# Kernel optimization log

Hardware: AMD Instinct MI355X
Metric: run time of the kernel (lower is better)

Reference implementation:

```python
import jax, jax.numpy as jnp
import numpy as np

THETA = 10000.0

def _rope(x, pos):
    # x: [b, h, s, hd]; pos: [s]
    hd = x.shape[-1]
    inv_freq = 1.0 / (THETA ** (jnp.arange(0, hd, 2, dtype=jnp.float32) / hd))  # [hd/2]
    ang = pos.astype(jnp.float32)[:, None] * inv_freq[None, :]                   # [s, hd/2]
    cos, sin = jnp.cos(ang), jnp.sin(ang)
    x1, x2 = x[..., 0::2], x[..., 1::2]
    r1 = x1 * cos - x2 * sin
    r2 = x1 * sin + x2 * cos
    return jnp.stack([r1, r2], axis=-1).reshape(x.shape)

def setup_inputs() -> dict:
    key = jax.random.key(0)
    ks = jax.random.split(key, 5)
    b, s, d = 2, 2048, 1024
    scale = 0.02
    return {
        "x": jax.random.normal(ks[0], (b, s, d), dtype=jnp.float32),
        "Wq": jax.random.normal(ks[1], (d, d), dtype=jnp.float32) * scale,
        "Wk": jax.random.normal(ks[2], (d, d), dtype=jnp.float32) * scale,
        "Wv": jax.random.normal(ks[3], (d, d), dtype=jnp.float32) * scale,
        "Wo": jax.random.normal(ks[4], (d, d), dtype=jnp.float32) * scale,
    }

def reference(x, Wq, Wk, Wv, Wo):
    b, s, d = x.shape
    n_heads = 16
    hd = d // n_heads

    def split_heads(t):  # [b,s,d] -> [b,h,s,hd]
        return t.reshape(b, s, n_heads, hd).transpose(0, 2, 1, 3)

    q = split_heads(x @ Wq.T)
    k = split_heads(x @ Wk.T)
    v = split_heads(x @ Wv.T)

    pos = jnp.arange(s)
    q = _rope(q, pos)
    k = _rope(k, pos)

    scores = jnp.einsum("bhqd,bhkd->bhqk", q, k) / jnp.sqrt(jnp.float32(hd))
    causal = jnp.tril(jnp.ones((s, s), dtype=bool))
    scores = jnp.where(causal, scores, -jnp.inf)
    attn = jax.nn.softmax(scores, axis=-1)
    ctx = jnp.einsum("bhqk,bhkd->bhqd", attn, v)
    ctx = ctx.transpose(0, 2, 1, 3).reshape(b, s, d)
    return ctx @ Wo.T
```

## Files before the change

kernel.cpp:

```cpp
#include <hip/hip_runtime.h>
#include <math.h>

#define B  2
#define S  2048
#define D  1024
#define NH 16
#define HD 64
#define NROWS (B * S)

#define AS1 __attribute__((address_space(1)))
#define AS3 __attribute__((address_space(3)))
#define GLD16(g, l) __builtin_amdgcn_global_load_lds((const AS1 void*)(g), (AS3 void*)(l), 16, 0, 0)

typedef __attribute__((ext_vector_type(8))) short short8;
typedef __attribute__((ext_vector_type(4))) float floatx4;

#define MFMA16(a, b, c) __builtin_amdgcn_mfma_f32_16x16x32_bf16((a), (b), (c), 0, 0, 0)

__device__ inline float fexp2(float x) { return __builtin_amdgcn_exp2f(x); }

__device__ inline unsigned short f2bf(float f) {
    union { float f; unsigned int u; } v; v.f = f;
    unsigned int u = v.u;
    u += 0x7fffu + ((u >> 16) & 1);
    return (unsigned short)(u >> 16);
}

__device__ inline unsigned int pack2bf(float a, float b) {
    unsigned int ua = __float_as_uint(a) + 0x8000u;
    unsigned int ub = __float_as_uint(b) + 0x8000u;
    return __builtin_amdgcn_perm(ub, ua, 0x07060302u);
}

__global__ __launch_bounds__(256) void cvt_kernel(
    const float* __restrict__ x,  const float* __restrict__ Wq,
    const float* __restrict__ Wk, const float* __restrict__ Wv,
    const float* __restrict__ Wo,
    unsigned short* __restrict__ xb,  unsigned short* __restrict__ wqb,
    unsigned short* __restrict__ wkb, unsigned short* __restrict__ wvb,
    unsigned short* __restrict__ wob, float2* __restrict__ tab)
{
    size_t idx = (size_t)blockIdx.x * 256 + threadIdx.x;
    if (idx >= (2u << 20)) {
        int tt = (int)(idx - (2u << 20));
        int j  = tt >> 9;
        int s0 = (tt & 511) << 2;
        float invf = fexp2(-(float)j * (13.287712379549449f / 32.0f));
        #pragma unroll
        for (int p = 0; p < 4; ++p) {
            float sn, cs;
            __sincosf((float)(s0 + p) * invf, &sn, &cs);
            tab[j * 2048 + s0 + p] = make_float2(cs, sn);
        }
        return;
    }
    const float* src; unsigned short* dst; size_t off;
    if (idx < (1u << 20)) { src = x; dst = xb; off = idx << 2; }
    else {
        size_t r = idx - (1u << 20);
        int w = (int)(r >> 18);
        off = (r & ((1u << 18) - 1)) << 2;
        src = (w == 0) ? Wq : (w == 1) ? Wk : (w == 2) ? Wv : Wo;
        dst = (w == 0) ? wqb : (w == 1) ? wkb : (w == 2) ? wvb : wob;
    }
    float4 f = *(const float4*)(src + off);
    ushort4 o;
    o.x = f2bf(f.x); o.y = f2bf(f.y); o.z = f2bf(f.z); o.w = f2bf(f.w);
    *(ushort4*)(dst + off) = o;
}

#define G2STAGE(Abase, Bbase, kk, AD, BD)                                      \
{                                                                              \
    GLD16(Abase + (size_t)rowS        * D + (kk) + koS, AD + t * 8);           \
    GLD16(Abase + (size_t)(rowS + 64) * D + (kk) + koS, AD + 2048 + t * 8);    \
    GLD16(Bbase + (size_t)rowS        * D + (kk) + koS, BD + t * 8);           \
    GLD16(Bbase + (size_t)(rowS + 64) * D + (kk) + koS, BD + 2048 + t * 8);    \
}

#define G2COMP(AC, BC)                                                         \
{                                                                              \
    short8 a[4], b[4];                                                         \
    _Pragma("unroll")                                                          \
    for (int mi = 0; mi < 4; ++mi)                                             \
        a[mi] = *(const short8*)&AC[(wr * 64 + mi * 16 + lm) * 32 + quad * 8]; \
    _Pragma("unroll")                                                          \
    for (int ni = 0; ni < 4; ++ni)                                             \
        b[ni] = *(const short8*)&BC[(wc * 64 + ni * 16 + lm) * 32 + quad * 8]; \
    _Pragma("unroll")                                                          \
    for (int mi = 0; mi < 4; ++mi)                                             \
        _Pragma("unroll")                                                      \
        for (int ni = 0; ni < 4; ++ni)                                         \
            acc[mi][ni] = MFMA16(b[ni], a[mi], acc[mi][ni]);      \
}

__global__ __launch_bounds__(256, 3) void gemm_qkv_mfma(
    const unsigned short* __restrict__ xb,
    const unsigned short* __restrict__ wqb,
    const unsigned short* __restrict__ wkb,
    const unsigned short* __restrict__ wvb,
    const float2* __restrict__ tab,
    unsigned short* __restrict__ Qo, unsigned short* __restrict__ Ko,
    unsigned short* __restrict__ Vo)
{
    __shared__ short As0[128 * 32];
    __shared__ short As1[128 * 32];
    __shared__ short Bs0[128 * 32];
    __shared__ short Bs1[128 * 32];

    const int t    = threadIdx.x;
    const int wave = t >> 6, lane = t & 63;
    const int lm   = lane & 15, quad = lane >> 4;
    const int wr   = wave >> 1, wc = wave & 1;
    const int rowS = t >> 2;
    const int koS  = (t & 3) << 3;

    const int i0  = blockIdx.x * 128;
    const int by  = blockIdx.y;
    const int mat = by >> 3;
    const int j0  = (by & 7) * 128;
    const unsigned short* __restrict__ W = (mat == 0) ? wqb : (mat == 1) ? wkb : wvb;
    unsigned short* __restrict__ out = (mat == 0) ? Qo : (mat == 1) ? Ko : Vo;

    const unsigned short* Abase = xb + (size_t)i0 * D;
    const unsigned short* Bbase = W  + (size_t)j0 * D;

    floatx4 acc[4][4] = {};

    G2STAGE(Abase, Bbase, 0, As0, Bs0);
    __syncthreads();
    for (int k0 = 0; k0 < D; k0 += 64) {
        G2STAGE(Abase, Bbase, k0 + 32, As1, Bs1);
        G2COMP(As0, Bs0);
        __syncthreads();
        if (k0 + 64 < D) G2STAGE(Abase, Bbase, k0 + 64, As0, Bs0);
        G2COMP(As1, Bs1);
        __syncthreads();
    }

    const int h = (j0 + wc * 64) >> 6;
    if (mat < 2) {
        #pragma unroll
        for (int mi = 0; mi < 4; ++mi) {
            const int mg = i0 + wr * 64 + mi * 16 + lm;
            const int si = mg & (S - 1), bb = mg >> 11;
            unsigned short* orow = out + ((size_t)(bb * NH + h) * S + si) * HD;
            #pragma unroll
            for (int ni = 0; ni < 4; ++ni) {
                const int dim0 = ni * 16 + quad * 4;
                const int j = dim0 >> 1;
                float2 t0 = tab[j * 2048 + si];
                float2 t1 = tab[(j + 1) * 2048 + si];
                floatx4 v = acc[mi][ni];
                float r0 = v[0] * t0.x - v[1] * t0.y;
                float r1 = v[0] * t0.y + v[1] * t0.x;
                float r2 = v[2] * t1.x - v[3] * t1.y;
                float r3 = v[2] * t1.y + v[3] * t1.x;
                if (mat == 0) {
                    r0 *= 0.1803368801111204f; r1 *= 0.1803368801111204f;
                    r2 *= 0.1803368801111204f; r3 *= 0.1803368801111204f;
                }
                ushort4 pk;
                pk.x = f2bf(r0); pk.y = f2bf(r1);
                pk.z = f2bf(r2); pk.w = f2bf(r3);
                *(ushort4*)(orow + dim0) = pk;
            }
        }
    } else {
        #pragma unroll
        for (int mi = 0; mi < 4; ++mi) {
            const int mg = i0 + wr * 64 + mi * 16 + lm;
            const int si = mg & (S - 1), bb = mg >> 11;
            unsigned short* vb = out + (size_t)(bb * NH + h) * HD * S + si;
            #pragma unroll
            for (int ni = 0; ni < 4; ++ni) {
                const int d0 = ni * 16 + quad * 4;
                #pragma unroll
                for (int p = 0; p < 4; ++p)
                    vb[(size_t)(d0 + p) * S] = f2bf(acc[mi][ni][p]);
            }
        }
    }
}

#define GSTAGE(Abase, Bbase, kk, AD, BD)                                       \
{                                                                              \
    GLD16(Abase + (size_t)rowA  * D + (kk) + koA,  AD + cA  * 8);              \
    GLD16(Bbase + (size_t)rowB0 * D + (kk) + koB0, BD + cB0 * 8);              \
    GLD16(Bbase + (size_t)rowB1 * D + (kk) + koB1, BD + cB1 * 8);              \
}

#define GCOMP(AC, BC)                                                          \
{                                                                              \
    short8 a[4], b[2];                                                         \
    _Pragma("unroll")                                                          \
    for (int mi = 0; mi < 4; ++mi)                                             \
        a[mi] = *(const short8*)&AC[(mi * 16 + lm) * 32 + quad * 8];           \
    _Pragma("unroll")                                                          \
    for (int ni = 0; ni < 2; ++ni)                                             \
        b[ni] = *(const short8*)&BC[(wave * 32 + ni * 16 + lm) * 32 + quad * 8]; \
    _Pragma("unroll")                                                          \
    for (int mi = 0; mi < 4; ++mi)                                             \
        _Pragma("unroll")                                                      \
        for (int ni = 0; ni < 2; ++ni)                                         \
            acc[mi][ni] = MFMA16(b[ni], a[mi], acc[mi][ni]);      \
}

#define GEMM_PREAMBLE                                                          \
    const int t    = threadIdx.x;                                              \
    const int wave = t >> 6, lane = t & 63;                                    \
    const int lm   = lane & 15, quad = lane >> 4;                              \
    const int cA   = wave * 64 + lane;                                         \
    const int rowA = cA >> 2,  koA  = (cA & 3) << 3;                           \
    const int cB0  = wave * 128 + lane;                                        \
    const int rowB0 = cB0 >> 2, koB0 = (cB0 & 3) << 3;                         \
    const int cB1  = cB0 + 64;                                                 \
    const int rowB1 = cB1 >> 2, koB1 = (cB1 & 3) << 3;

#define GEMM_KLOOP(Abase, Bbase)                                               \
    GSTAGE(Abase, Bbase, 0, As0, Bs0);                                         \
    __syncthreads();                                                           \
    for (int k0 = 0; k0 < D; k0 += 64) {                                       \
        GSTAGE(Abase, Bbase, k0 + 32, As1, Bs1);                               \
        GCOMP(As0, Bs0);                                                       \
        __syncthreads();                                                       \
        if (k0 + 64 < D) GSTAGE(Abase, Bbase, k0 + 64, As0, Bs0);              \
        GCOMP(As1, Bs1);                                                       \
        __syncthreads();                                                       \
    }

__global__ __launch_bounds__(256) void gemm_out_mfma(
    const unsigned short* __restrict__ Cb,
    const unsigned short* __restrict__ wob,
    float* __restrict__ out)
{
    __shared__ short As0[64 * 32];
    __shared__ short As1[64 * 32];
    __shared__ short Bs0[128 * 32];
    __shared__ short Bs1[128 * 32];

    GEMM_PREAMBLE
    const int i0 = blockIdx.x * 64;
    const int j0 = blockIdx.y * 128;

    const unsigned short* Abase = Cb  + (size_t)i0 * D;
    const unsigned short* Bbase = wob + (size_t)j0 * D;

    floatx4 acc[4][2] = {};
    GEMM_KLOOP(Abase, Bbase)

    #pragma unroll
    for (int mi = 0; mi < 4; ++mi) {
        const int mg = i0 + mi * 16 + lm;
        float* orow = out + (size_t)mg * D;
        #pragma unroll
        for (int ni = 0; ni < 2; ++ni) {
            const int ng = j0 + wave * 32 + ni * 16 + quad * 4;
            *(floatx4*)(orow + ng) = acc[mi][ni];
        }
    }
}

#define ATTN_STEP(KC, VC, KN, VN)                                              \
{                                                                              \
    _Pragma("unroll")                                                          \
    for (int i = 0; i < 2; ++i) {                                              \
        int c = t + i * 256;                                                   \
        int row = c >> 3;                                                      \
        int dkc = (c & 7) ^ (row & 7);                                         \
        GLD16(Kg + (size_t)(k0n + row) * HD + dkc * 8, &KN[0][0] + c * 8);     \
        GLD16(Vg + (size_t)row * S + k0n + dkc * 8,    &VN[0][0] + c * 8);     \
    }                                                                          \
    short8 kb0[4], kb1[4];                                                     \
    _Pragma("unroll")                                                          \
    for (int nt = 0; nt < 4; ++nt) {                                           \
        kb0[nt] = *(const short8*)&KC[nt * 16 + lm][(quad ^ sw) * 8];          \
        kb1[nt] = *(const short8*)&KC[nt * 16 + lm][((4 + quad) ^ sw) * 8];    \
    }                                                                          \
    floatx4 sc[4];                                                             \
    _Pragma("unroll")                                                          \
    for (int nt = 0; nt < 4; ++nt) {                                           \
        floatx4 s = {0.f, 0.f, 0.f, 0.f};                                      \
        s = MFMA16(kb0[nt], qa0, s);                \
        s = MFMA16(kb1[nt], qa1, s);                                           \
        sc[nt] = s;                                                            \
    }                                                                          \
    if (diag) {                                                                \
        _Pragma("unroll")                                                      \
        for (int nt = 0; nt < 4; ++nt)                                         \
            _Pragma("unroll")                                                  \
            for (int r = 0; r < 4; ++r) {                                      \
                float pe = fexp2(sc[nt][r]);                                   \
                if (nt * 16 + quad * 4 + r > 16 * wave + lm) pe = 0.0f;        \
                sc[nt][r] = pe;                                                \
                lsum += pe;                                                    \
            }                                                                  \
    } else {                                                                   \
        _Pragma("unroll")                                                      \
        for (int nt = 0; nt < 4; ++nt)                                         \
            _Pragma("unroll")                                                  \
            for (int r = 0; r < 4; ++r) {                                      \
                float pe = fexp2(sc[nt][r]);                                   \
                sc[nt][r] = pe;                                                \
                lsum += pe;                                                    \
            }                                                                  \
    }                                                                          \
    _Pragma("unroll")                                                          \
    for (int nt = 0; nt < 4; ++nt) {                                           \
        uint2 pk;                                                              \
        pk.x = pack2bf(sc[nt][0], sc[nt][1]);                                  \
        pk.y = pack2bf(sc[nt][2], sc[nt][3]);                                  \
        int cp = (nt * 4 + quad) ^ psw;                                        \
        *(uint2*)&Ps[16 * wave + lm][cp * 4] = pk;                             \
    }                                                                          \
    short8 pa0 = *(const short8*)&Ps[16 * wave + lm][((quad * 2) ^ psw) * 4];  \
    short8 pa1 = *(const short8*)&Ps[16 * wave + lm][((8 + quad * 2) ^ psw) * 4]; \
    _Pragma("unroll")                                                          \
    for (int nt = 0; nt < 4; ++nt) {                                           \
        short8 vb0 = *(const short8*)&VC[nt * 16 + lm][(quad ^ sw) * 8];       \
        short8 vb1 = *(const short8*)&VC[nt * 16 + lm][((4 + quad) ^ sw) * 8]; \
        o[nt] = MFMA16(pa0, vb0, o[nt]);                                       \
        o[nt] = MFMA16(pa1, vb1, o[nt]);                                       \
    }                                                                          \
    __syncthreads();                                                           \
}

__global__ __launch_bounds__(256, 4) void attn_mfma(
    const unsigned short* __restrict__ Qb,
    const unsigned short* __restrict__ Kb,
    const unsigned short* __restrict__ Vt,
    unsigned short* __restrict__ Cb)
{
    __shared__ unsigned short Ks0[64][64];
    __shared__ unsigned short Ks1[64][64];
    __shared__ unsigned short Vs0[64][64];
    __shared__ unsigned short Vs1[64][64];
    __shared__ unsigned short Ps[64][64];

    const int t    = threadIdx.x;
    const int lane = t & 63, wave = t >> 6;
    const int lm   = lane & 15, quad = lane >> 4;
    const int sw   = lm & 7;
    const int psw  = (lm & 7) << 1;

    const int b     = blockIdx.x;
    const int bh    = b & 31;
    const int f     = (b >> 5) & 7;
    const int round = b >> 8;
    int qt;
    if      (round == 0) qt = f;
    else if (round == 1) qt = 15 - f;
    else if (round == 2) qt = 16 + f;
    else                 qt = 31 - f;
    const int q0 = qt * 64;

    const unsigned short* Qg = Qb + (size_t)bh * S * HD;
    const unsigned short* Kg = Kb + (size_t)bh * S * HD;
    const unsigned short* Vg = Vt + (size_t)bh * HD * S;

    short8 qa0 = *(const short8*)(Qg + (size_t)(q0 + 16 * wave + lm) * HD + quad * 8);
    short8 qa1 = *(const short8*)(Qg + (size_t)(q0 + 16 * wave + lm) * HD + 32 + quad * 8);

    #pragma unroll
    for (int i = 0; i < 2; ++i) {
        int c = t + i * 256;
        int row = c >> 3;
        int dkc = (c & 7) ^ (row & 7);
        GLD16(Kg + (size_t)row * HD + dkc * 8, &Ks0[0][0] + c * 8);
        GLD16(Vg + (size_t)row * S + dkc * 8,  &Vs0[0][0] + c * 8);
    }

    float lsum = 0.0f;
    floatx4 o[4] = {};

    __syncthreads();

    for (int kt = 0; kt <= qt; ++kt) {
        const int k0n = (kt + 1) * 64;
        const bool diag = (kt == qt);
        if ((kt & 1) == 0) ATTN_STEP(Ks0, Vs0, Ks1, Vs1)
        else               ATTN_STEP(Ks1, Vs1, Ks0, Vs0)
    }

    lsum += __shfl_xor(lsum, 16);
    lsum += __shfl_xor(lsum, 32);
    const int h = bh & (NH - 1), bb = bh >> 4;
    #pragma unroll
    for (int r = 0; r < 4; ++r) {
        float lr  = __shfl(lsum, (wave << 6 | (quad * 4 + r)) & 63);
        float inv = 1.0f / lr;
        size_t row = (size_t)bb * S + q0 + 16 * wave + quad * 4 + r;
        #pragma unroll
        for (int nt = 0; nt < 4; ++nt)
            Cb[row * D + h * HD + nt * 16 + lm] = f2bf(o[nt][r] * inv);
    }
}

extern "C" void kernel_launch(void* const* d_in, const int* in_sizes, int n_in,
                              void* d_out, int out_size, void* d_ws, size_t ws_size,
                              hipStream_t stream) {
    (void)in_sizes; (void)n_in; (void)out_size; (void)ws_size;
    const float* x  = (const float*)d_in[0];
    const float* Wq = (const float*)d_in[1];
    const float* Wk = (const float*)d_in[2];
    const float* Wv = (const float*)d_in[3];
    const float* Wo = (const float*)d_in[4];
    float* out = (float*)d_out;

    char* w = (char*)d_ws;
    unsigned short* Qb  = (unsigned short*)(w);
    unsigned short* Kb  = (unsigned short*)(w + (((size_t)8)  << 20));
    unsigned short* Vtb = (unsigned short*)(w + (((size_t)16) << 20));
    unsigned short* Cb  = (unsigned short*)(w + (((size_t)24) << 20));
    unsigned short* xb  = (unsigned short*)(w + (((size_t)32) << 20));
    unsigned short* wqb = (unsigned short*)(w + (((size_t)40) << 20));
    unsigned short* wkb = (unsigned short*)(w + (((size_t)42) << 20));
    unsigned short* wvb = (unsigned short*)(w + (((size_t)44) << 20));
    unsigned short* wob = (unsigned short*)(w + (((size_t)46) << 20));
    float2*         tab = (float2*)(w + (((size_t)48) << 20));

    cvt_kernel<<<8256, 256, 0, stream>>>(x, Wq, Wk, Wv, Wo,
                                         xb, wqb, wkb, wvb, wob, tab);

    dim3 g1(NROWS / 128, 24);
    gemm_qkv_mfma<<<g1, 256, 0, stream>>>(xb, wqb, wkb, wvb, tab, Qb, Kb, Vtb);

    attn_mfma<<<1024, 256, 0, stream>>>(Qb, Kb, Vtb, Cb);

    dim3 g3(NROWS / 64, D / 128);
    gemm_out_mfma<<<g3, 256, 0, stream>>>(Cb, wob, out);
}
```

Before: 168.6 us.

## Double attention query tile to 128 rows per block for K/V reuse

Each attention block now handles 128 query rows (two 16-row slices per wave) instead of 64, so every K/V tile loaded into shared memory feeds twice as many MFMAs. The grid halves to 512 blocks, the P buffer doubles, and launch bounds drop to 2 blocks per CU to allow more registers for the doubled accumulators. The risks are lower occupancy, fewer blocks for load balancing across the causal triangle, and a diagonal region that now spans two K tiles with extra masking work.

```diff
diff --git a/kernel.cpp b/kernel.cpp
--- a/kernel.cpp
+++ b/kernel.cpp
@@ -270,61 +270,78 @@
         GLD16(Kg + (size_t)(k0n + row) * HD + dkc * 8, &KN[0][0] + c * 8);     \
         GLD16(Vg + (size_t)row * S + k0n + dkc * 8,    &VN[0][0] + c * 8);     \
     }                                                                          \
-    short8 kb0[4], kb1[4];                                                     \
-    _Pragma("unroll")                                                          \
-    for (int nt = 0; nt < 4; ++nt) {                                           \
-        kb0[nt] = *(const short8*)&KC[nt * 16 + lm][(quad ^ sw) * 8];          \
-        kb1[nt] = *(const short8*)&KC[nt * 16 + lm][((4 + quad) ^ sw) * 8];    \
-    }                                                                          \
-    floatx4 sc[4];                                                             \
-    _Pragma("unroll")                                                          \
-    for (int nt = 0; nt < 4; ++nt) {                                           \
-        floatx4 s = {0.f, 0.f, 0.f, 0.f};                                      \
-        s = MFMA16(kb0[nt], qa0, s);                \
-        s = MFMA16(kb1[nt], qa1, s);                                           \
-        sc[nt] = s;                                                            \
+    floatx4 sc[2][4];                                                          \
+    {                                                                          \
+        short8 kb0[4], kb1[4];                                                 \
+        _Pragma("unroll")                                                      \
+        for (int nt = 0; nt < 4; ++nt) {                                       \
+            kb0[nt] = *(const short8*)&KC[nt * 16 + lm][(quad ^ sw) * 8];      \
+            kb1[nt] = *(const short8*)&KC[nt * 16 + lm][((4 + quad) ^ sw) * 8];\
+        }                                                                      \
+        _Pragma("unroll")                                                      \
+        for (int qs = 0; qs < 2; ++qs)                                         \
+            _Pragma("unroll")                                                  \
+            for (int nt = 0; nt < 4; ++nt) {                                   \
+                floatx4 s = {0.f, 0.f, 0.f, 0.f};                              \
+                s = MFMA16(kb0[nt], qa0[qs], s);     \
+                s = MFMA16(kb1[nt], qa1[qs], s);                               \
+                sc[qs][nt] = s;                                                \
+            }                                                                  \
     }                                                                          \
     if (diag) {                                                                \
         _Pragma("unroll")                                                      \
-        for (int nt = 0; nt < 4; ++nt)                                         \
+        for (int qs = 0; qs < 2; ++qs)                                         \
             _Pragma("unroll")                                                  \
-            for (int r = 0; r < 4; ++r) {                                      \
-                float pe = fexp2(sc[nt][r]);                                   \
-                if (nt * 16 + quad * 4 + r > 16 * wave + lm) pe = 0.0f;        \
-                sc[nt][r] = pe;                                                \
-                lsum += pe;                                                    \
-            }                                                                  \
+            for (int nt = 0; nt < 4; ++nt)                                     \
+                _Pragma("unroll")                                              \
+                for (int r = 0; r < 4; ++r) {                                  \
+                    float pe = fexp2(sc[qs][nt][r]);                           \
+                    if (nt * 16 + quad * 4 + r > rel + qs * 16) pe = 0.0f;     \
+                    sc[qs][nt][r] = pe;                                        \
+                    lsum[qs] += pe;                                            \
+                }                                                              \
     } else {                                                                   \
         _Pragma("unroll")                                                      \
-        for (int nt = 0; nt < 4; ++nt)                                         \
+        for (int qs = 0; qs < 2; ++qs)                                         \
             _Pragma("unroll")                                                  \
-            for (int r = 0; r < 4; ++r) {                                      \
-                float pe = fexp2(sc[nt][r]);                                   \
-                sc[nt][r] = pe;                                                \
-                lsum += pe;                                                    \
-            }                                                                  \
+            for (int nt = 0; nt < 4; ++nt)                                     \
+                _Pragma("unroll")                                              \
+                for (int r = 0; r < 4; ++r) {                                  \
+                    float pe = fexp2(sc[qs][nt][r]);                           \
+                    sc[qs][nt][r] = pe;                                        \
+                    lsum[qs] += pe;                                            \
+                }                                                              \
     }                                                                          \
     _Pragma("unroll")                                                          \
-    for (int nt = 0; nt < 4; ++nt) {                                           \
-        uint2 pk;                                                              \
-        pk.x = pack2bf(sc[nt][0], sc[nt][1]);                                  \
-        pk.y = pack2bf(sc[nt][2], sc[nt][3]);                                  \
-        int cp = (nt * 4 + quad) ^ psw;                                        \
-        *(uint2*)&Ps[16 * wave + lm][cp * 4] = pk;                             \
+    for (int qs = 0; qs < 2; ++qs)                                             \
+        _Pragma("unroll")                                                      \
+        for (int nt = 0; nt < 4; ++nt) {                                       \
+            uint2 pk;                                                          \
+            pk.x = pack2bf(sc[qs][nt][0], sc[qs][nt][1]);                      \
+            pk.y = pack2bf(sc[qs][nt][2], sc[qs][nt][3]);                      \
+            int cp = (nt * 4 + quad) ^ psw;                                    \
+            *(uint2*)&Ps[wave * 32 + qs * 16 + lm][cp * 4] = pk;               \
+        }                                                                      \
+    short8 pa[2][2];                                                           \
+    _Pragma("unroll")                                                          \
+    for (int qs = 0; qs < 2; ++qs) {                                           \
+        pa[qs][0] = *(const short8*)&Ps[wave * 32 + qs * 16 + lm][((quad * 2) ^ psw) * 4];     \
+        pa[qs][1] = *(const short8*)&Ps[wave * 32 + qs * 16 + lm][((8 + quad * 2) ^ psw) * 4]; \
     }                                                                          \
-    short8 pa0 = *(const short8*)&Ps[16 * wave + lm][((quad * 2) ^ psw) * 4];  \
-    short8 pa1 = *(const short8*)&Ps[16 * wave + lm][((8 + quad * 2) ^ psw) * 4]; \
     _Pragma("unroll")                                                          \
     for (int nt = 0; nt < 4; ++nt) {                                           \
         short8 vb0 = *(const short8*)&VC[nt * 16 + lm][(quad ^ sw) * 8];       \
         short8 vb1 = *(const short8*)&VC[nt * 16 + lm][((4 + quad) ^ sw) * 8]; \
-        o[nt] = MFMA16(pa0, vb0, o[nt]);                                       \
-        o[nt] = MFMA16(pa1, vb1, o[nt]);                                       \
+        _Pragma("unroll")                                                      \
+        for (int qs = 0; qs < 2; ++qs) {                                       \
+            o[qs][nt] = MFMA16(pa[qs][0], vb0, o[qs][nt]);                     \
+            o[qs][nt] = MFMA16(pa[qs][1], vb1, o[qs][nt]);                     \
+        }                                                                      \
     }                                                                          \
     __syncthreads();                                                           \
 }
 
-__global__ __launch_bounds__(256, 4) void attn_mfma(
+__global__ __launch_bounds__(256, 2) void attn_mfma(
     const unsigned short* __restrict__ Qb,
     const unsigned short* __restrict__ Kb,
     const unsigned short* __restrict__ Vt,
@@ -334,7 +351,7 @@
     __shared__ unsigned short Ks1[64][64];
     __shared__ unsigned short Vs0[64][64];
     __shared__ unsigned short Vs1[64][64];
-    __shared__ unsigned short Ps[64][64];
+    __shared__ unsigned short Ps[128][64];
 
     const int t    = threadIdx.x;
     const int lane = t & 63, wave = t >> 6;
@@ -346,19 +363,21 @@
     const int bh    = b & 31;
     const int f     = (b >> 5) & 7;
     const int round = b >> 8;
-    int qt;
-    if      (round == 0) qt = f;
-    else if (round == 1) qt = 15 - f;
-    else if (round == 2) qt = 16 + f;
-    else                 qt = 31 - f;
-    const int q0 = qt * 64;
+    const int qt    = (round == 0) ? f : 15 - f;
+    const int q0    = qt * 128;
+    const int nkv   = 2 * qt + 2;
 
     const unsigned short* Qg = Qb + (size_t)bh * S * HD;
     const unsigned short* Kg = Kb + (size_t)bh * S * HD;
     const unsigned short* Vg = Vt + (size_t)bh * HD * S;
 
-    short8 qa0 = *(const short8*)(Qg + (size_t)(q0 + 16 * wave + lm) * HD + quad * 8);
-    short8 qa1 = *(const short8*)(Qg + (size_t)(q0 + 16 * wave + lm) * HD + 32 + quad * 8);
+    short8 qa0[2], qa1[2];
+    #pragma unroll
+    for (int qs = 0; qs < 2; ++qs) {
+        const unsigned short* qrow = Qg + (size_t)(q0 + wave * 32 + qs * 16 + lm) * HD;
+        qa0[qs] = *(const short8*)(qrow + quad * 8);
+        qa1[qs] = *(const short8*)(qrow + 32 + quad * 8);
+    }
 
     #pragma unroll
     for (int i = 0; i < 2; ++i) {
@@ -369,29 +388,37 @@
         GLD16(Vg + (size_t)row * S + dkc * 8,  &Vs0[0][0] + c * 8);
     }
 
-    float lsum = 0.0f;
-    floatx4 o[4] = {};
+    float lsum[2] = {0.f, 0.f};
+    floatx4 o[2][4] = {};
+    const int qbase = q0 + wave * 32 + lm;
 
     __syncthreads();
 
-    for (int kt = 0; kt <= qt; ++kt) {
-        const int k0n = (kt + 1) * 64;
-        const bool diag = (kt == qt);
+    for (int kt = 0; kt < nkv; ++kt) {
+        const int k0n  = (kt + 1) * 64;
+        const bool diag = (kt >= nkv - 2);
+        const int rel  = qbase - kt * 64;
         if ((kt & 1) == 0) ATTN_STEP(Ks0, Vs0, Ks1, Vs1)
         else               ATTN_STEP(Ks1, Vs1, Ks0, Vs0)
     }
 
-    lsum += __shfl_xor(lsum, 16);
-    lsum += __shfl_xor(lsum, 32);
+    #pragma unroll
+    for (int qs = 0; qs < 2; ++qs) {
+        lsum[qs] += __shfl_xor(lsum[qs], 16);
+        lsum[qs] += __shfl_xor(lsum[qs], 32);
+    }
     const int h = bh & (NH - 1), bb = bh >> 4;
     #pragma unroll
-    for (int r = 0; r < 4; ++r) {
-        float lr  = __shfl(lsum, (wave << 6 | (quad * 4 + r)) & 63);
-        float inv = 1.0f / lr;
-        size_t row = (size_t)bb * S + q0 + 16 * wave + quad * 4 + r;
+    for (int qs = 0; qs < 2; ++qs) {
         #pragma unroll
-        for (int nt = 0; nt < 4; ++nt)
-            Cb[row * D + h * HD + nt * 16 + lm] = f2bf(o[nt][r] * inv);
+        for (int r = 0; r < 4; ++r) {
+            float lr  = __shfl(lsum[qs], quad * 4 + r);
+            float inv = 1.0f / lr;
+            size_t row = (size_t)bb * S + q0 + wave * 32 + qs * 16 + quad * 4 + r;
+            #pragma unroll
+            for (int nt = 0; nt < 4; ++nt)
+                Cb[row * D + h * HD + nt * 16 + lm] = f2bf(o[qs][nt][r] * inv);
+        }
     }
 }
 
@@ -424,7 +451,7 @@
     dim3 g1(NROWS / 128, 24);
     gemm_qkv_mfma<<<g1, 256, 0, stream>>>(xb, wqb, wkb, wvb, tab, Qb, Kb, Vtb);
 
-    attn_mfma<<<1024, 256, 0, stream>>>(Qb, Kb, Vtb, Cb);
+    attn_mfma<<<512, 256, 0, stream>>>(Qb, Kb, Vtb, Cb);
 
     dim3 g3(NROWS / 64, D / 128);
     gemm_out_mfma<<<g3, 256, 0, stream>>>(Cb, wob, out);
```

New measurement: 171.5 us. Within noise of the previous version (+1.7%).

## Enlarge QKV GEMM tiles to 256x256 with swizzled LDS and explicit waits

Applied to the files above, without the earlier changes.

Rewrites the QKV projection GEMM to use 256x256 output tiles with 512 threads and a K-step of 64. The LDS layout uses an XOR swizzle to avoid bank conflicts, and a double-buffered pipeline is paced by explicit vmcnt waits and raw barriers. Wave priority is raised around the MFMA block. Each block now gets more operand reuse, but the grid shrinks to 192 blocks with about 128KB of LDS each, so not every CU gets a block and occupancy drops.

```diff
diff --git a/kernel.cpp b/kernel.cpp
--- a/kernel.cpp
+++ b/kernel.cpp
@@ -69,31 +69,42 @@
     *(ushort4*)(dst + off) = o;
 }
 
-#define G2STAGE(Abase, Bbase, kk, AD, BD)                                      \
+#define SWAIT(n) asm volatile("s_waitcnt vmcnt(" n ")" ::: "memory")
+
+#define STAGE8(p, kk)                                                          \
 {                                                                              \
-    GLD16(Abase + (size_t)rowS        * D + (kk) + koS, AD + t * 8);           \
-    GLD16(Abase + (size_t)(rowS + 64) * D + (kk) + koS, AD + 2048 + t * 8);    \
-    GLD16(Bbase + (size_t)rowS        * D + (kk) + koS, BD + t * 8);           \
-    GLD16(Bbase + (size_t)(rowS + 64) * D + (kk) + koS, BD + 2048 + t * 8);    \
-}
-
-#define G2COMP(AC, BC)                                                         \
+    _Pragma("unroll")                                                          \
+    for (int hh = 0; hh < 2; ++hh) {                                           \
+        _Pragma("unroll")                                                      \
+        for (int jj = 0; jj < 2; ++jj) {                                       \
+            const int idx = jj * 512 + t;                                      \
+            const int row = hh * 128 + (idx >> 3);                             \
+            const int ch  = (idx & 7) ^ (row & 7);                             \
+            GLD16(Ab + (size_t)row * D + (kk) + ch * 8, &As[p][hh * 8192 + idx * 8]); \
+            GLD16(Bb + (size_t)row * D + (kk) + ch * 8, &Bs[p][hh * 8192 + idx * 8]); \
+        }                                                                      \
+    }                                                                          \
+}
+
+#define QCOMP(p, ks)                                                           \
 {                                                                              \
-    short8 a[4], b[4];                                                         \
-    _Pragma("unroll")                                                          \
-    for (int mi = 0; mi < 4; ++mi)                                             \
-        a[mi] = *(const short8*)&AC[(wr * 64 + mi * 16 + lm) * 32 + quad * 8]; \
+    short8 a[8], b[4];                                                         \
+    _Pragma("unroll")                                                          \
+    for (int mi = 0; mi < 8; ++mi)                                             \
+        a[mi] = *(const short8*)&As[p][(wr * 128 + mi * 16 + lm) * 64 + (((ks) * 4 + quad) ^ sw) * 8]; \
     _Pragma("unroll")                                                          \
     for (int ni = 0; ni < 4; ++ni)                                             \
-        b[ni] = *(const short8*)&BC[(wc * 64 + ni * 16 + lm) * 32 + quad * 8]; \
-    _Pragma("unroll")                                                          \
-    for (int mi = 0; mi < 4; ++mi)                                             \
+        b[ni] = *(const short8*)&Bs[p][(wc * 64 + ni * 16 + lm) * 64 + (((ks) * 4 + quad) ^ sw) * 8]; \
+    __builtin_amdgcn_s_setprio(1);                                             \
+    _Pragma("unroll")                                                          \
+    for (int mi = 0; mi < 8; ++mi)                                             \
         _Pragma("unroll")                                                      \
         for (int ni = 0; ni < 4; ++ni)                                         \
             acc[mi][ni] = MFMA16(b[ni], a[mi], acc[mi][ni]);      \
-}
-
-__global__ __launch_bounds__(256, 3) void gemm_qkv_mfma(
+    __builtin_amdgcn_s_setprio(0);                                             \
+}
+
+__global__ __launch_bounds__(512, 2) void gemm_qkv_mfma(
     const unsigned short* __restrict__ xb,
     const unsigned short* __restrict__ wqb,
     const unsigned short* __restrict__ wkb,
@@ -102,46 +113,50 @@
     unsigned short* __restrict__ Qo, unsigned short* __restrict__ Ko,
     unsigned short* __restrict__ Vo)
 {
-    __shared__ short As0[128 * 32];
-    __shared__ short As1[128 * 32];
-    __shared__ short Bs0[128 * 32];
-    __shared__ short Bs1[128 * 32];
+    __shared__ short As[2][256 * 64];
+    __shared__ short Bs[2][256 * 64];
 
     const int t    = threadIdx.x;
-    const int wave = t >> 6, lane = t & 63;
+    const int wid  = t >> 6, lane = t & 63;
     const int lm   = lane & 15, quad = lane >> 4;
-    const int wr   = wave >> 1, wc = wave & 1;
-    const int rowS = t >> 2;
-    const int koS  = (t & 3) << 3;
-
-    const int i0  = blockIdx.x * 128;
+    const int wr   = wid >> 2, wc = wid & 3;
+    const int sw   = lm & 7;
+
+    const int i0  = blockIdx.x * 256;
     const int by  = blockIdx.y;
-    const int mat = by >> 3;
-    const int j0  = (by & 7) * 128;
+    const int mat = by >> 2;
+    const int j0  = (by & 3) * 256;
     const unsigned short* __restrict__ W = (mat == 0) ? wqb : (mat == 1) ? wkb : wvb;
     unsigned short* __restrict__ out = (mat == 0) ? Qo : (mat == 1) ? Ko : Vo;
 
-    const unsigned short* Abase = xb + (size_t)i0 * D;
-    const unsigned short* Bbase = W  + (size_t)j0 * D;
-
-    floatx4 acc[4][4] = {};
-
-    G2STAGE(Abase, Bbase, 0, As0, Bs0);
-    __syncthreads();
-    for (int k0 = 0; k0 < D; k0 += 64) {
-        G2STAGE(Abase, Bbase, k0 + 32, As1, Bs1);
-        G2COMP(As0, Bs0);
-        __syncthreads();
-        if (k0 + 64 < D) G2STAGE(Abase, Bbase, k0 + 64, As0, Bs0);
-        G2COMP(As1, Bs1);
-        __syncthreads();
-    }
-
-    const int h = (j0 + wc * 64) >> 6;
+    const unsigned short* Ab = xb + (size_t)i0 * D;
+    const unsigned short* Bb = W  + (size_t)j0 * D;
+
+    floatx4 acc[8][4] = {};
+
+    STAGE8(0, 0);
+    for (int kt = 0; kt < 16; ++kt) {
+        const int p = kt & 1;
+        if (kt < 15) {
+            STAGE8(p ^ 1, (kt + 1) * 64);
+            SWAIT("8");
+        } else {
+            SWAIT("0");
+        }
+        __builtin_amdgcn_sched_barrier(0);
+        __builtin_amdgcn_s_barrier();
+        __builtin_amdgcn_sched_barrier(0);
+        QCOMP(p, 0);
+        QCOMP(p, 1);
+        __builtin_amdgcn_sched_barrier(0);
+        __builtin_amdgcn_s_barrier();
+    }
+
+    const int h = (j0 >> 6) + wc;
     if (mat < 2) {
         #pragma unroll
-        for (int mi = 0; mi < 4; ++mi) {
-            const int mg = i0 + wr * 64 + mi * 16 + lm;
+        for (int mi = 0; mi < 8; ++mi) {
+            const int mg = i0 + wr * 128 + mi * 16 + lm;
             const int si = mg & (S - 1), bb = mg >> 11;
             unsigned short* orow = out + ((size_t)(bb * NH + h) * S + si) * HD;
             #pragma unroll
@@ -167,8 +182,8 @@
         }
     } else {
         #pragma unroll
-        for (int mi = 0; mi < 4; ++mi) {
-            const int mg = i0 + wr * 64 + mi * 16 + lm;
+        for (int mi = 0; mi < 8; ++mi) {
+            const int mg = i0 + wr * 128 + mi * 16 + lm;
             const int si = mg & (S - 1), bb = mg >> 11;
             unsigned short* vb = out + (size_t)(bb * NH + h) * HD * S + si;
             #pragma unroll
@@ -421,8 +436,8 @@
     cvt_kernel<<<8256, 256, 0, stream>>>(x, Wq, Wk, Wv, Wo,
                                          xb, wqb, wkb, wvb, wob, tab);
 
-    dim3 g1(NROWS / 128, 24);
-    gemm_qkv_mfma<<<g1, 256, 0, stream>>>(xb, wqb, wkb, wvb, tab, Qb, Kb, Vtb);
+    dim3 g1(NROWS / 256, 12);
+    gemm_qkv_mfma<<<g1, 512, 0, stream>>>(xb, wqb, wkb, wvb, tab, Qb, Kb, Vtb);
 
     attn_mfma<<<1024, 256, 0, stream>>>(Qb, Kb, Vtb, Cb);
 
```

Result: slower. 176.7 us (+4.8%).
